# Kernel optimization log

Measured on AMD Instinct MI355X. Metric: run time of the kernel, lower is better.

## Reference

```python
import jax, jax.numpy as jnp
import numpy as np

B, S, IK, IV = 16, 2048, 3, 1
D = IK + IV          # input_size = 4
H = 256              # hidden_size
F = 512              # dim_feedforward
L = 2                # num_layers
EPS = 1e-5


def setup_inputs() -> dict:
    key = jax.random.key(0)
    ks = jax.random.split(key, 16)
    n = jax.random.normal
    inp = {
        'KEY': n(ks[0], (B, S, IK), jnp.float32),
        'VALUE': n(ks[1], (B, S, IV), jnp.float32),
        # per-layer kernel-attention projections (stacked on layer axis)
        'Wq': n(ks[2], (L, D, H), jnp.float32) * 0.1,
        'bq': jnp.zeros((L, H), jnp.float32),
        'Wk': n(ks[3], (L, D, H), jnp.float32) * 0.1,
        'bk': jnp.zeros((L, H), jnp.float32),
        'Wv': n(ks[4], (L, D, H), jnp.float32) * 0.1,
        'bv': jnp.zeros((L, H), jnp.float32),
        'Wo': n(ks[5], (L, H, D), jnp.float32) * 0.1,
        'bo': jnp.zeros((L, D), jnp.float32),
        'bw': jnp.ones((L,), jnp.float32),          # Gaussian kernel bandwidth
        # LayerNorm 1
        'g1': jnp.ones((L, D), jnp.float32),
        'be1': jnp.zeros((L, D), jnp.float32),
        # FFN
        'W1': n(ks[6], (L, D, F), jnp.float32) * 0.1,
        'b1': jnp.zeros((L, F), jnp.float32),
        'W2': n(ks[7], (L, F, D), jnp.float32) * 0.1,
        'b2': jnp.zeros((L, D), jnp.float32),
        # LayerNorm 2
        'g2': jnp.ones((L, D), jnp.float32),
        'be2': jnp.zeros((L, D), jnp.float32),
        # final fc: input_size -> input_v
        'Wfc': n(ks[8], (D, IV), jnp.float32) * 0.1,
        'bfc': jnp.zeros((IV,), jnp.float32),
    }
    return inp


def _layernorm(x, g, b):
    m = x.mean(-1, keepdims=True)
    v = ((x - m) ** 2).mean(-1, keepdims=True)
    return (x - m) * jax.lax.rsqrt(v + EPS) * g + b


def reference(KEY, VALUE, Wq, bq, Wk, bk, Wv, bv, Wo, bo, bw,
              g1, be1, W1, b1, W2, b2, g2, be2, Wfc, bfc):
    # positioning: concat coords and values -> [B, S, D]
    X = jnp.concatenate([KEY, VALUE], axis=-1)
    n_layers = Wq.shape[0]
    for i in range(n_layers):
        # Nadaraya-Watson Gaussian kernel attention (madsnn, type='nwd', kernel='gauss')
        Q = X @ Wq[i] + bq[i]                      # [B,S,H]
        K = X @ Wk[i] + bk[i]                      # [B,S,H]
        V = X @ Wv[i] + bv[i]                      # [B,S,H]
        # pairwise squared distances ||q-k||^2, [B,S,S]
        d2 = ((Q * Q).sum(-1)[:, :, None]
              + (K * K).sum(-1)[:, None, :]
              - 2.0 * jnp.einsum('bqh,bkh->bqk', Q, K))
        attn = jax.nn.softmax(-0.5 * d2 * (bw[i] ** 2), axis=-1)
        attn_out = jnp.einsum('bqk,bkh->bqh', attn, V) @ Wo[i] + bo[i]  # [B,S,D]
        # residual + LayerNorm + FFN + residual + LayerNorm (dropout = identity in eval)
        res = _layernorm(X + attn_out, g1[i], be1[i])
        ff = jax.nn.relu(res @ W1[i] + b1[i]) @ W2[i] + b2[i]
        X = _layernorm(res + ff, g2[i], be2[i])
    return X @ Wfc + bfc                            # [B,S,IV]
```

## Files before the change

### kernel.cpp

```cpp
#include <hip/hip_runtime.h>

#define BB 16
#define SS 2048
#define NTOK (BB*SS)
#define NPAIR (NTOK/2)
#define PLANE (NPAIR*4)
#define FF 512
#define EPSF 1e-5f
#define QW 8

#if __has_builtin(__builtin_amdgcn_exp2f)
#define EXP2F(x) __builtin_amdgcn_exp2f(x)
#else
#define EXP2F(x) exp2f(x)
#endif

typedef float v2f __attribute__((ext_vector_type(2)));


__device__ __forceinline__ float wred64(float v) {
#pragma unroll
  for (int m = 32; m > 0; m >>= 1) v += __shfl_xor(v, m, 64);
  return v;
}

__device__ __forceinline__ float rflf(float v) {
  union { float f; int i; } u; u.f = v;
  u.i = __builtin_amdgcn_readfirstlane(u.i);
  return u.f;
}


__global__ __launch_bounds__(64) void prep_kernel(
    const float* __restrict__ Wq, const float* __restrict__ bq,
    const float* __restrict__ Wk, const float* __restrict__ bk,
    const float* __restrict__ Wv, const float* __restrict__ bv,
    const float* __restrict__ Wo, const float* __restrict__ bw,
    const float* __restrict__ W1, const float* __restrict__ b1,
    const float* __restrict__ W2,
    float* __restrict__ sm, float* __restrict__ w1t)
{
  const int i = blockIdx.x;
  const int lane = threadIdx.x;
  float m4[4][4] = {{0}}, gkk[4][4] = {{0}}, wvo[4][4] = {{0}};
  float akk[4] = {0}, bvo[4] = {0};
  float ck1 = 0.f, ck2 = 0.f;

  for (int h = lane; h < 256; h += 64) {
    float vq[4], vk[4], vv[4], wo4[4];
#pragma unroll
    for (int a = 0; a < 4; ++a) {
      vq[a]  = Wq[(i*4 + a)*256 + h];
      vk[a]  = Wk[(i*4 + a)*256 + h];
      vv[a]  = Wv[(i*4 + a)*256 + h];
      wo4[a] = Wo[(i*256 + h)*4 + a];
    }
    const float bqh = bq[i*256 + h], bkh = bk[i*256 + h], bvh = bv[i*256 + h];
#pragma unroll
    for (int a = 0; a < 4; ++a) {
#pragma unroll
      for (int c = 0; c < 4; ++c) {
        m4[a][c]  = fmaf(vq[a], vk[c], m4[a][c]);
        gkk[a][c] = fmaf(vk[a], vk[c], gkk[a][c]);
        wvo[a][c] = fmaf(vv[a], wo4[c], wvo[a][c]);
      }
      akk[a] = fmaf(vk[a], bqh - bkh, akk[a]);
      bvo[a] = fmaf(bvh, wo4[a], bvo[a]);
    }
    ck1 = fmaf(bqh, bkh, ck1);
    ck2 = fmaf(bkh, bkh, ck2);
  }
#pragma unroll
  for (int a = 0; a < 4; ++a) {
#pragma unroll
    for (int c = 0; c < 4; ++c) {
      m4[a][c]  = wred64(m4[a][c]);
      gkk[a][c] = wred64(gkk[a][c]);
      wvo[a][c] = wred64(wvo[a][c]);
    }
    akk[a] = wred64(akk[a]);
    bvo[a] = wred64(bvo[a]);
  }
  ck1 = wred64(ck1); ck2 = wred64(ck2);

  if (lane == 0) {
    const float bwv = bw[i];
    const float bw2 = bwv * bwv * 1.44269504088896f;
    float* s = sm + i*64;
#pragma unroll
    for (int a = 0; a < 4; ++a) {
#pragma unroll
      for (int c = 0; c < 4; ++c) {
        s[a*4+c]      = bw2 * m4[a][c];
        s[16 + a*4+c] = -0.5f * bw2 * gkk[a][c];
        s[32 + a*4+c] = wvo[a][c];
      }
      s[48+a] = bw2 * akk[a];
      s[52+a] = bvo[a];
    }
    s[56] = bw2 * (ck1 - 0.5f * ck2);
  }
  for (int f = lane; f < FF; f += 64) {
    float* rec = w1t + (i*FF + f)*12;
#pragma unroll
    for (int c = 0; c < 4; ++c) rec[c]   = W1[(i*4 + c)*FF + f];
#pragma unroll
    for (int c = 0; c < 4; ++c) rec[4+c] = W2[(i*FF + f)*4 + c];
    rec[8] = b1[i*FF + f];
    rec[9] = 0.f; rec[10] = 0.f; rec[11] = 0.f;
  }
}

__device__ __forceinline__ void compute_feat(const float x[4], const float* __restrict__ s,
                                             float* __restrict__ featrec)
{
  float P[4], VT[4], tk[4];
#pragma unroll
  for (int a = 0; a < 4; ++a) {
    P[a]  = fmaf(s[a*4+3], x[3], fmaf(s[a*4+2], x[2], fmaf(s[a*4+1], x[1], s[a*4+0]*x[0])));
    tk[a] = fmaf(s[16+a*4+3], x[3], fmaf(s[16+a*4+2], x[2], fmaf(s[16+a*4+1], x[1], s[16+a*4+0]*x[0])));
    VT[a] = s[52+a] + fmaf(s[32+3*4+a], x[3], fmaf(s[32+2*4+a], x[2], fmaf(s[32+1*4+a], x[1], s[32+0*4+a]*x[0])));
  }
  float R = s[56];
#pragma unroll
  for (int a = 0; a < 4; ++a) R = fmaf(tk[a] + s[48+a], x[a], R);
  featrec[0]=P[0]; featrec[1]=P[1]; featrec[2]=P[2]; featrec[3]=P[3];
  featrec[4]=VT[0]; featrec[5]=VT[1]; featrec[6]=VT[2]; featrec[7]=VT[3];
  featrec[8]=R;
}

__global__ __launch_bounds__(256) void feat_kernel(
    const float* __restrict__ KEY, const float* __restrict__ VALUE,
    const float* __restrict__ sm, float* __restrict__ feat)
{
  const int p = blockIdx.x*256 + threadIdx.x;
  const int ta = 2*p, tb = 2*p + 1;
  float xa[4] = {KEY[ta*3], KEY[ta*3+1], KEY[ta*3+2], VALUE[ta]};
  float xb[4] = {KEY[tb*3], KEY[tb*3+1], KEY[tb*3+2], VALUE[tb]};
  float fa[9], fb[9];
  compute_feat(xa, sm, fa);
  compute_feat(xb, sm, fb);
#pragma unroll
  for (int pl = 0; pl < 4; ++pl) {
    *(float4*)(feat + (size_t)pl*PLANE + (size_t)p*4) =
        make_float4(fa[2*pl], fb[2*pl], fa[2*pl+1], fb[2*pl+1]);
  }
  *(float4*)(feat + (size_t)4*PLANE + (size_t)p*4) =
      make_float4(fa[8], fb[8], 0.f, 0.f);
}

__device__ __forceinline__ void ln4(const float t[4], const float* __restrict__ g,
                                    const float* __restrict__ b, float r[4])
{
  const float m = 0.25f*(t[0]+t[1]+t[2]+t[3]);
  const float d0 = t[0]-m, d1 = t[1]-m, d2 = t[2]-m, d3 = t[3]-m;
  const float v = 0.25f*(d0*d0 + d1*d1 + d2*d2 + d3*d3);
  const float sc = rsqrtf(v + EPSF);
  r[0] = fmaf(d0*sc, g[0], b[0]);
  r[1] = fmaf(d1*sc, g[1], b[1]);
  r[2] = fmaf(d2*sc, g[2], b[2]);
  r[3] = fmaf(d3*sc, g[3], b[3]);
}

__global__ __launch_bounds__(256, 4) void layer_kernel(
    const float* __restrict__ KEY, const float* __restrict__ VALUE,
    const float* __restrict__ X, const float* __restrict__ feat,
    const float* __restrict__ w1t, const float* __restrict__ smn,
    const float* __restrict__ bo, const float* __restrict__ g1, const float* __restrict__ be1,
    const float* __restrict__ b2v, const float* __restrict__ g2, const float* __restrict__ be2,
    float* __restrict__ Xout, float* __restrict__ featout,
    const float* __restrict__ Wfc, const float* __restrict__ bfc,
    float* __restrict__ outp, int first, int last)
{
  const int bid = blockIdx.x;
  const int b = bid >> 6, qg = bid & 63;
  const int qbase = (b << 11) + (qg << 5);
  const int tid = threadIdx.x;
  const int lane = tid & 63, wv = tid >> 6;
  const int q0 = qbase + wv*QW;

  __shared__ float sums[4*QW*9];
  __shared__ float ress[32*4];
  __shared__ float redf[8*32*4];

  float qx0[QW], qx1[QW], qx2[QW], qx3[QW];
#pragma unroll
  for (int q = 0; q < QW; ++q) {
    const int gq = q0 + q;
    float a, b_, c, d;
    if (first) {
      a = KEY[gq*3]; b_ = KEY[gq*3+1]; c = KEY[gq*3+2]; d = VALUE[gq];
    } else {
      const float4 xv = *(const float4*)(X + (size_t)gq*4);
      a = xv.x; b_ = xv.y; c = xv.z; d = xv.w;
    }
    qx0[q] = rflf(a); qx1[q] = rflf(b_); qx2[q] = rflf(c); qx3[q] = rflf(d);
  }

  v2f aV0[QW], aV1[QW], aV2[QW], aV3[QW], aD[QW];
#pragma unroll
  for (int q = 0; q < QW; ++q) {
    aV0[q] = v2f{0.f,0.f}; aV1[q] = v2f{0.f,0.f};
    aV2[q] = v2f{0.f,0.f}; aV3[q] = v2f{0.f,0.f};
    aD[q]  = v2f{0.f,0.f};
  }

  const int pb = (b << 10) + lane;
#pragma unroll 4
  for (int it = 0; it < 16; ++it) {
    const size_t o = (size_t)(pb + (it << 6)) * 4;
    const float4 A  = *(const float4*)(feat + o);
    const float4 Bf = *(const float4*)(feat + (size_t)PLANE + o);
    const float4 C  = *(const float4*)(feat + (size_t)2*PLANE + o);
    const float4 D  = *(const float4*)(feat + (size_t)3*PLANE + o);
    const float4 E  = *(const float4*)(feat + (size_t)4*PLANE + o);
    const v2f P0 = v2f{A.x, A.y},   P1 = v2f{A.z, A.w};
    const v2f P2 = v2f{Bf.x, Bf.y}, P3 = v2f{Bf.z, Bf.w};
    const v2f V0 = v2f{C.x, C.y},   V1 = v2f{C.z, C.w};
    const v2f V2 = v2f{D.x, D.y},   V3 = v2f{D.z, D.w};
    const v2f Rp = v2f{E.x, E.y};
#pragma unroll
    for (int q = 0; q < QW; ++q) {
      v2f l = __builtin_elementwise_fma(P0, v2f{qx0[q], qx0[q]}, Rp);
      l = __builtin_elementwise_fma(P1, v2f{qx1[q], qx1[q]}, l);
      l = __builtin_elementwise_fma(P2, v2f{qx2[q], qx2[q]}, l);
      l = __builtin_elementwise_fma(P3, v2f{qx3[q], qx3[q]}, l);
      const v2f e = v2f{EXP2F(l.x), EXP2F(l.y)};
      aV0[q] = __builtin_elementwise_fma(e, V0, aV0[q]);
      aV1[q] = __builtin_elementwise_fma(e, V1, aV1[q]);
      aV2[q] = __builtin_elementwise_fma(e, V2, aV2[q]);
      aV3[q] = __builtin_elementwise_fma(e, V3, aV3[q]);
      aD[q] += e;
    }
  }

  float s[QW][5];
#pragma unroll
  for (int q = 0; q < QW; ++q) {
    s[q][0] = aV0[q].x + aV0[q].y;
    s[q][1] = aV1[q].x + aV1[q].y;
    s[q][2] = aV2[q].x + aV2[q].y;
    s[q][3] = aV3[q].x + aV3[q].y;
    s[q][4] = aD[q].x + aD[q].y;
  }
#pragma unroll
  for (int q = 0; q < QW; ++q)
#pragma unroll
    for (int c = 0; c < 5; ++c) s[q][c] = wred64(s[q][c]);

  if (lane == 0) {
    float* dst = sums + wv*(QW*9);
#pragma unroll
    for (int q = 0; q < QW; ++q) {
#pragma unroll
      for (int c = 0; c < 5; ++c) dst[q*9 + c] = s[q][c];
    }
  }
  __syncthreads();

  if (tid < 32) {
    const float* sv = sums + tid*9;
    const float inv = 1.0f / sv[4];
    const int gq = qbase + tid;
    float xv0, xv1, xv2, xv3;
    if (first) {
      xv0 = KEY[gq*3]; xv1 = KEY[gq*3+1]; xv2 = KEY[gq*3+2]; xv3 = VALUE[gq];
    } else {
      const float4 xv = *(const float4*)(X + (size_t)gq*4);
      xv0 = xv.x; xv1 = xv.y; xv2 = xv.z; xv3 = xv.w;
    }
    float t4[4];
    t4[0] = xv0 + fmaf(sv[0], inv, bo[0]);
    t4[1] = xv1 + fmaf(sv[1], inv, bo[1]);
    t4[2] = xv2 + fmaf(sv[2], inv, bo[2]);
    t4[3] = xv3 + fmaf(sv[3], inv, bo[3]);
    float r[4];
    ln4(t4, g1, be1, r);
    *(float4*)(ress + tid*4) = make_float4(r[0], r[1], r[2], r[3]);
  }
  __syncthreads();

  const int tok = tid & 31, fc = tid >> 5;
  const float4 rv = *(const float4*)(ress + tok*4);
  float fa0 = 0.f, fa1 = 0.f, fa2 = 0.f, fa3 = 0.f;
  const float* wt = w1t + (size_t)fc*64*12;
#pragma unroll 4
  for (int f = 0; f < 64; ++f) {
    const float* rec = wt + f*12;
    const float4 w1r = *(const float4*)rec;
    const float4 w2r = *(const float4*)(rec + 4);
    const float b1f = rec[8];
    float h = fmaf(rv.w, w1r.w, fmaf(rv.z, w1r.z, fmaf(rv.y, w1r.y, fmaf(rv.x, w1r.x, b1f))));
    h = fmaxf(h, 0.f);
    fa0 = fmaf(h, w2r.x, fa0);
    fa1 = fmaf(h, w2r.y, fa1);
    fa2 = fmaf(h, w2r.z, fa2);
    fa3 = fmaf(h, w2r.w, fa3);
  }
  *(float4*)(redf + (size_t)((fc << 5) + tok)*4) = make_float4(fa0, fa1, fa2, fa3);
  __syncthreads();

  if (tid < 32) {
    float t2[4];
#pragma unroll
    for (int c = 0; c < 4; ++c) {
      float sa = b2v[c];
#pragma unroll
      for (int k = 0; k < 8; ++k) sa += redf[(size_t)((k << 5) + tid)*4 + c];
      t2[c] = ress[tid*4 + c] + sa;
    }
    float y[4];
    ln4(t2, g2, be2, y);
    const int gq = qbase + tid;
    if (last) {
      outp[gq] = fmaf(y[3], Wfc[3], fmaf(y[2], Wfc[2], fmaf(y[1], Wfc[1], fmaf(y[0], Wfc[0], bfc[0]))));
    } else {
      *(float4*)(Xout + (size_t)gq*4) = make_float4(y[0], y[1], y[2], y[3]);
      float fr[9];
      compute_feat(y, smn, fr);
      const int p = gq >> 1, par = gq & 1;
#pragma unroll
      for (int c = 0; c < 8; ++c)
        featout[(size_t)(c >> 1)*PLANE + (size_t)p*4 + (c & 1)*2 + par] = fr[c];
      featout[(size_t)4*PLANE + (size_t)p*4 + par] = fr[8];
    }
  }
}

extern "C" void kernel_launch(void* const* d_in, const int* in_sizes, int n_in,
                              void* d_out, int out_size, void* d_ws, size_t ws_size,
                              hipStream_t stream)
{
  const float* KEY   = (const float*)d_in[0];
  const float* VALUE = (const float*)d_in[1];
  const float* Wq  = (const float*)d_in[2];
  const float* bq  = (const float*)d_in[3];
  const float* Wk  = (const float*)d_in[4];
  const float* bk  = (const float*)d_in[5];
  const float* Wv  = (const float*)d_in[6];
  const float* bv  = (const float*)d_in[7];
  const float* Wo  = (const float*)d_in[8];
  const float* bo  = (const float*)d_in[9];
  const float* bw  = (const float*)d_in[10];
  const float* g1  = (const float*)d_in[11];
  const float* be1 = (const float*)d_in[12];
  const float* W1  = (const float*)d_in[13];
  const float* b1  = (const float*)d_in[14];
  const float* W2  = (const float*)d_in[15];
  const float* b2  = (const float*)d_in[16];
  const float* g2  = (const float*)d_in[17];
  const float* be2 = (const float*)d_in[18];
  const float* Wfc = (const float*)d_in[19];
  const float* bfc = (const float*)d_in[20];
  float* out = (float*)d_out;

  float* w    = (float*)d_ws;
  float* sm   = w;
  float* w1t  = w + 128;
  float* X1   = w + 12416;
  float* f0   = w + 143488;
  float* f1   = w + 471168;

  prep_kernel<<<2, 64, 0, stream>>>(Wq, bq, Wk, bk, Wv, bv, Wo, bw,
                                    W1, b1, W2, sm, w1t);
  feat_kernel<<<64, 256, 0, stream>>>(KEY, VALUE, sm, f0);

  layer_kernel<<<1024, 256, 0, stream>>>(KEY, VALUE, X1, f0,
      w1t, sm + 64,
      bo, g1, be1, b2, g2, be2,
      X1, f1, Wfc, bfc, out, 1, 0);

  layer_kernel<<<1024, 256, 0, stream>>>(KEY, VALUE, X1, f1,
      w1t + FF*12, sm,
      bo + 4, g1 + 4, be1 + 4, b2 + 4, g2 + 4, be2 + 4,
      X1, f1, Wfc, bfc, out, 0, 1);
}
```

Measured before the change: 187.2 us.

## Store raw key coordinates and fold projections into query side and epilogue

```diff
diff --git a/kernel.cpp b/kernel.cpp
--- a/kernel.cpp
+++ b/kernel.cpp
@@ -4,10 +4,9 @@
 #define SS 2048
 #define NTOK (BB*SS)
 #define NPAIR (NTOK/2)
-#define PLANE (NPAIR*4)
 #define FF 512
 #define EPSF 1e-5f
-#define QW 8
+#define QW 4
 
 #if __has_builtin(__builtin_amdgcn_exp2f)
 #define EXP2F(x) __builtin_amdgcn_exp2f(x)
@@ -111,42 +110,31 @@
   }
 }
 
-__device__ __forceinline__ void compute_feat(const float x[4], const float* __restrict__ s,
-                                             float* __restrict__ featrec)
-{
-  float P[4], VT[4], tk[4];
+__device__ __forceinline__ float compute_R(const float x[4], const float* __restrict__ s)
+{
+  float R = s[56];
 #pragma unroll
   for (int a = 0; a < 4; ++a) {
-    P[a]  = fmaf(s[a*4+3], x[3], fmaf(s[a*4+2], x[2], fmaf(s[a*4+1], x[1], s[a*4+0]*x[0])));
-    tk[a] = fmaf(s[16+a*4+3], x[3], fmaf(s[16+a*4+2], x[2], fmaf(s[16+a*4+1], x[1], s[16+a*4+0]*x[0])));
-    VT[a] = s[52+a] + fmaf(s[32+3*4+a], x[3], fmaf(s[32+2*4+a], x[2], fmaf(s[32+1*4+a], x[1], s[32+0*4+a]*x[0])));
-  }
-  float R = s[56];
-#pragma unroll
-  for (int a = 0; a < 4; ++a) R = fmaf(tk[a] + s[48+a], x[a], R);
-  featrec[0]=P[0]; featrec[1]=P[1]; featrec[2]=P[2]; featrec[3]=P[3];
-  featrec[4]=VT[0]; featrec[5]=VT[1]; featrec[6]=VT[2]; featrec[7]=VT[3];
-  featrec[8]=R;
+    const float tk = fmaf(s[16+a*4+3], x[3], fmaf(s[16+a*4+2], x[2],
+                     fmaf(s[16+a*4+1], x[1], s[16+a*4+0]*x[0])));
+    R = fmaf(tk + s[48+a], x[a], R);
+  }
+  return R;
 }
 
 __global__ __launch_bounds__(256) void feat_kernel(
     const float* __restrict__ KEY, const float* __restrict__ VALUE,
-    const float* __restrict__ sm, float* __restrict__ feat)
+    const float* __restrict__ sm,
+    float* __restrict__ fXA, float* __restrict__ fXB, float* __restrict__ fRR)
 {
   const int p = blockIdx.x*256 + threadIdx.x;
   const int ta = 2*p, tb = 2*p + 1;
   float xa[4] = {KEY[ta*3], KEY[ta*3+1], KEY[ta*3+2], VALUE[ta]};
   float xb[4] = {KEY[tb*3], KEY[tb*3+1], KEY[tb*3+2], VALUE[tb]};
-  float fa[9], fb[9];
-  compute_feat(xa, sm, fa);
-  compute_feat(xb, sm, fb);
-#pragma unroll
-  for (int pl = 0; pl < 4; ++pl) {
-    *(float4*)(feat + (size_t)pl*PLANE + (size_t)p*4) =
-        make_float4(fa[2*pl], fb[2*pl], fa[2*pl+1], fb[2*pl+1]);
-  }
-  *(float4*)(feat + (size_t)4*PLANE + (size_t)p*4) =
-      make_float4(fa[8], fb[8], 0.f, 0.f);
+  const float Ra = compute_R(xa, sm), Rb = compute_R(xb, sm);
+  *(float4*)(fXA + (size_t)p*4) = make_float4(xa[0], xb[0], xa[1], xb[1]);
+  *(float4*)(fXB + (size_t)p*4) = make_float4(xa[2], xb[2], xa[3], xb[3]);
+  *(v2f*)(fRR + (size_t)p*2) = v2f{Ra, Rb};
 }
 
 __device__ __forceinline__ void ln4(const float t[4], const float* __restrict__ g,
@@ -162,13 +150,15 @@
   r[3] = fmaf(d3*sc, g[3], b[3]);
 }
 
-__global__ __launch_bounds__(256, 4) void layer_kernel(
+__global__ __launch_bounds__(512, 8) void layer_kernel(
     const float* __restrict__ KEY, const float* __restrict__ VALUE,
-    const float* __restrict__ X, const float* __restrict__ feat,
-    const float* __restrict__ w1t, const float* __restrict__ smn,
+    const float* __restrict__ X,
+    const float* __restrict__ fXA, const float* __restrict__ fXB, const float* __restrict__ fRR,
+    const float* __restrict__ w1t, const float* __restrict__ smc, const float* __restrict__ smn,
     const float* __restrict__ bo, const float* __restrict__ g1, const float* __restrict__ be1,
     const float* __restrict__ b2v, const float* __restrict__ g2, const float* __restrict__ be2,
-    float* __restrict__ Xout, float* __restrict__ featout,
+    float* __restrict__ Xout,
+    float* __restrict__ foXA, float* __restrict__ foXB, float* __restrict__ foRR,
     const float* __restrict__ Wfc, const float* __restrict__ bfc,
     float* __restrict__ outp, int first, int last)
 {
@@ -179,88 +169,108 @@
   const int lane = tid & 63, wv = tid >> 6;
   const int q0 = qbase + wv*QW;
 
-  __shared__ float sums[4*QW*9];
-  __shared__ float ress[32*4];
-  __shared__ float redf[8*32*4];
-
-  float qx0[QW], qx1[QW], qx2[QW], qx3[QW];
+  __shared__ float smem[5120];
+  float* sXA = smem;
+  float* sXB = smem + 2048;
+  float* sRR = smem + 4096;
+  float* sums = smem;
+  float* ress = smem + 256;
+  float* redf = smem + 512;
+
+  float gv0[QW], gv1[QW], gv2[QW], gv3[QW];
 #pragma unroll
   for (int q = 0; q < QW; ++q) {
     const int gq = q0 + q;
-    float a, b_, c, d;
+    float x0, x1, x2, x3;
     if (first) {
-      a = KEY[gq*3]; b_ = KEY[gq*3+1]; c = KEY[gq*3+2]; d = VALUE[gq];
+      x0 = KEY[gq*3]; x1 = KEY[gq*3+1]; x2 = KEY[gq*3+2]; x3 = VALUE[gq];
     } else {
       const float4 xv = *(const float4*)(X + (size_t)gq*4);
-      a = xv.x; b_ = xv.y; c = xv.z; d = xv.w;
-    }
-    qx0[q] = rflf(a); qx1[q] = rflf(b_); qx2[q] = rflf(c); qx3[q] = rflf(d);
-  }
-
-  v2f aV0[QW], aV1[QW], aV2[QW], aV3[QW], aD[QW];
+      x0 = xv.x; x1 = xv.y; x2 = xv.z; x3 = xv.w;
+    }
+    float g0 = fmaf(smc[12], x3, fmaf(smc[ 8], x2, fmaf(smc[4], x1, smc[0]*x0)));
+    float g1_ = fmaf(smc[13], x3, fmaf(smc[ 9], x2, fmaf(smc[5], x1, smc[1]*x0)));
+    float g2_ = fmaf(smc[14], x3, fmaf(smc[10], x2, fmaf(smc[6], x1, smc[2]*x0)));
+    float g3_ = fmaf(smc[15], x3, fmaf(smc[11], x2, fmaf(smc[7], x1, smc[3]*x0)));
+    gv0[q] = rflf(g0); gv1[q] = rflf(g1_); gv2[q] = rflf(g2_); gv3[q] = rflf(g3_);
+  }
+
+  v2f aX0[QW], aX1[QW], aX2[QW], aX3[QW], aD[QW];
 #pragma unroll
   for (int q = 0; q < QW; ++q) {
-    aV0[q] = v2f{0.f,0.f}; aV1[q] = v2f{0.f,0.f};
-    aV2[q] = v2f{0.f,0.f}; aV3[q] = v2f{0.f,0.f};
+    aX0[q] = v2f{0.f,0.f}; aX1[q] = v2f{0.f,0.f};
+    aX2[q] = v2f{0.f,0.f}; aX3[q] = v2f{0.f,0.f};
     aD[q]  = v2f{0.f,0.f};
   }
 
-  const int pb = (b << 10) + lane;
-#pragma unroll 4
-  for (int it = 0; it < 16; ++it) {
-    const size_t o = (size_t)(pb + (it << 6)) * 4;
-    const float4 A  = *(const float4*)(feat + o);
-    const float4 Bf = *(const float4*)(feat + (size_t)PLANE + o);
-    const float4 C  = *(const float4*)(feat + (size_t)2*PLANE + o);
-    const float4 D  = *(const float4*)(feat + (size_t)3*PLANE + o);
-    const float4 E  = *(const float4*)(feat + (size_t)4*PLANE + o);
-    const v2f P0 = v2f{A.x, A.y},   P1 = v2f{A.z, A.w};
-    const v2f P2 = v2f{Bf.x, Bf.y}, P3 = v2f{Bf.z, Bf.w};
-    const v2f V0 = v2f{C.x, C.y},   V1 = v2f{C.z, C.w};
-    const v2f V2 = v2f{D.x, D.y},   V3 = v2f{D.z, D.w};
-    const v2f Rp = v2f{E.x, E.y};
+  const int pbb = b << 10;
+#pragma unroll
+  for (int c = 0; c < 2; ++c) {
+    {
+      const int gp = pbb + c*512 + tid;
+      const float4 va = *(const float4*)(fXA + (size_t)gp*4);
+      const float4 vb = *(const float4*)(fXB + (size_t)gp*4);
+      const v2f    vr = *(const v2f*)(fRR + (size_t)gp*2);
+      __syncthreads();
+      *(float4*)(sXA + tid*4) = va;
+      *(float4*)(sXB + tid*4) = vb;
+      *(v2f*)(sRR + tid*2) = vr;
+      __syncthreads();
+    }
+#pragma unroll 2
+    for (int it = 0; it < 8; ++it) {
+      const int p = lane + (it << 6);
+      const float4 XAv = *(const float4*)(sXA + p*4);
+      const float4 XBv = *(const float4*)(sXB + p*4);
+      const v2f   RRv = *(const v2f*)(sRR + p*2);
+      const v2f X0 = v2f{XAv.x, XAv.y}, X1 = v2f{XAv.z, XAv.w};
+      const v2f X2 = v2f{XBv.x, XBv.y}, X3 = v2f{XBv.z, XBv.w};
+#pragma unroll
+      for (int q = 0; q < QW; ++q) {
+        v2f l = __builtin_elementwise_fma(X0, v2f{gv0[q], gv0[q]}, RRv);
+        l = __builtin_elementwise_fma(X1, v2f{gv1[q], gv1[q]}, l);
+        l = __builtin_elementwise_fma(X2, v2f{gv2[q], gv2[q]}, l);
+        l = __builtin_elementwise_fma(X3, v2f{gv3[q], gv3[q]}, l);
+        const v2f e = v2f{EXP2F(l.x), EXP2F(l.y)};
+        aX0[q] = __builtin_elementwise_fma(e, X0, aX0[q]);
+        aX1[q] = __builtin_elementwise_fma(e, X1, aX1[q]);
+        aX2[q] = __builtin_elementwise_fma(e, X2, aX2[q]);
+        aX3[q] = __builtin_elementwise_fma(e, X3, aX3[q]);
+        aD[q] += e;
+      }
+    }
+  }
+  __syncthreads();
+
+  {
+    float s[QW][5];
 #pragma unroll
     for (int q = 0; q < QW; ++q) {
-      v2f l = __builtin_elementwise_fma(P0, v2f{qx0[q], qx0[q]}, Rp);
-      l = __builtin_elementwise_fma(P1, v2f{qx1[q], qx1[q]}, l);
-      l = __builtin_elementwise_fma(P2, v2f{qx2[q], qx2[q]}, l);
-      l = __builtin_elementwise_fma(P3, v2f{qx3[q], qx3[q]}, l);
-      const v2f e = v2f{EXP2F(l.x), EXP2F(l.y)};
-      aV0[q] = __builtin_elementwise_fma(e, V0, aV0[q]);
-      aV1[q] = __builtin_elementwise_fma(e, V1, aV1[q]);
-      aV2[q] = __builtin_elementwise_fma(e, V2, aV2[q]);
-      aV3[q] = __builtin_elementwise_fma(e, V3, aV3[q]);
-      aD[q] += e;
-    }
-  }
-
-  float s[QW][5];
-#pragma unroll
-  for (int q = 0; q < QW; ++q) {
-    s[q][0] = aV0[q].x + aV0[q].y;
-    s[q][1] = aV1[q].x + aV1[q].y;
-    s[q][2] = aV2[q].x + aV2[q].y;
-    s[q][3] = aV3[q].x + aV3[q].y;
-    s[q][4] = aD[q].x + aD[q].y;
-  }
-#pragma unroll
-  for (int q = 0; q < QW; ++q)
-#pragma unroll
-    for (int c = 0; c < 5; ++c) s[q][c] = wred64(s[q][c]);
-
-  if (lane == 0) {
-    float* dst = sums + wv*(QW*9);
-#pragma unroll
-    for (int q = 0; q < QW; ++q) {
-#pragma unroll
-      for (int c = 0; c < 5; ++c) dst[q*9 + c] = s[q][c];
+      s[q][0] = aX0[q].x + aX0[q].y;
+      s[q][1] = aX1[q].x + aX1[q].y;
+      s[q][2] = aX2[q].x + aX2[q].y;
+      s[q][3] = aX3[q].x + aX3[q].y;
+      s[q][4] = aD[q].x + aD[q].y;
+    }
+#pragma unroll
+    for (int q = 0; q < QW; ++q)
+#pragma unroll
+      for (int c = 0; c < 5; ++c) s[q][c] = wred64(s[q][c]);
+    if (lane == 0) {
+#pragma unroll
+      for (int q = 0; q < QW; ++q) {
+        float* dst = sums + (wv*QW + q)*6;
+#pragma unroll
+        for (int c = 0; c < 5; ++c) dst[c] = s[q][c];
+      }
     }
   }
   __syncthreads();
 
   if (tid < 32) {
-    const float* sv = sums + tid*9;
+    const float* sv = sums + tid*6;
     const float inv = 1.0f / sv[4];
+    const float m0 = sv[0]*inv, m1 = sv[1]*inv, m2 = sv[2]*inv, m3 = sv[3]*inv;
     const int gq = qbase + tid;
     float xv0, xv1, xv2, xv3;
     if (first) {
@@ -270,10 +280,16 @@
       xv0 = xv.x; xv1 = xv.y; xv2 = xv.z; xv3 = xv.w;
     }
     float t4[4];
-    t4[0] = xv0 + fmaf(sv[0], inv, bo[0]);
-    t4[1] = xv1 + fmaf(sv[1], inv, bo[1]);
-    t4[2] = xv2 + fmaf(sv[2], inv, bo[2]);
-    t4[3] = xv3 + fmaf(sv[3], inv, bo[3]);
+#pragma unroll
+    for (int a = 0; a < 4; ++a) {
+      float at = smc[52+a];
+      at = fmaf(smc[32+0*4+a], m0, at);
+      at = fmaf(smc[32+1*4+a], m1, at);
+      at = fmaf(smc[32+2*4+a], m2, at);
+      at = fmaf(smc[32+3*4+a], m3, at);
+      const float xr = (a==0) ? xv0 : (a==1) ? xv1 : (a==2) ? xv2 : xv3;
+      t4[a] = xr + at + bo[a];
+    }
     float r[4];
     ln4(t4, g1, be1, r);
     *(float4*)(ress + tid*4) = make_float4(r[0], r[1], r[2], r[3]);
@@ -283,9 +299,9 @@
   const int tok = tid & 31, fc = tid >> 5;
   const float4 rv = *(const float4*)(ress + tok*4);
   float fa0 = 0.f, fa1 = 0.f, fa2 = 0.f, fa3 = 0.f;
-  const float* wt = w1t + (size_t)fc*64*12;
+  const float* wt = w1t + (size_t)fc*32*12;
 #pragma unroll 4
-  for (int f = 0; f < 64; ++f) {
+  for (int f = 0; f < 32; ++f) {
     const float* rec = wt + f*12;
     const float4 w1r = *(const float4*)rec;
     const float4 w2r = *(const float4*)(rec + 4);
@@ -306,7 +322,7 @@
     for (int c = 0; c < 4; ++c) {
       float sa = b2v[c];
 #pragma unroll
-      for (int k = 0; k < 8; ++k) sa += redf[(size_t)((k << 5) + tid)*4 + c];
+      for (int k = 0; k < 16; ++k) sa += redf[(size_t)((k << 5) + tid)*4 + c];
       t2[c] = ress[tid*4 + c] + sa;
     }
     float y[4];
@@ -316,13 +332,13 @@
       outp[gq] = fmaf(y[3], Wfc[3], fmaf(y[2], Wfc[2], fmaf(y[1], Wfc[1], fmaf(y[0], Wfc[0], bfc[0]))));
     } else {
       *(float4*)(Xout + (size_t)gq*4) = make_float4(y[0], y[1], y[2], y[3]);
-      float fr[9];
-      compute_feat(y, smn, fr);
+      const float Rn = compute_R(y, smn);
       const int p = gq >> 1, par = gq & 1;
-#pragma unroll
-      for (int c = 0; c < 8; ++c)
-        featout[(size_t)(c >> 1)*PLANE + (size_t)p*4 + (c & 1)*2 + par] = fr[c];
-      featout[(size_t)4*PLANE + (size_t)p*4 + par] = fr[8];
+      foXA[(size_t)p*4 + par]     = y[0];
+      foXA[(size_t)p*4 + 2 + par] = y[1];
+      foXB[(size_t)p*4 + par]     = y[2];
+      foXB[(size_t)p*4 + 2 + par] = y[3];
+      foRR[(size_t)p*2 + par]     = Rn;
     }
   }
 }
@@ -358,20 +374,24 @@
   float* sm   = w;
   float* w1t  = w + 128;
   float* X1   = w + 12416;
-  float* f0   = w + 143488;
-  float* f1   = w + 471168;
+  float* f0XA = w + 143488;
+  float* f0XB = w + 209024;
+  float* f0RR = w + 274560;
+  float* f1XA = w + 307328;
+  float* f1XB = w + 372864;
+  float* f1RR = w + 438400;
 
   prep_kernel<<<2, 64, 0, stream>>>(Wq, bq, Wk, bk, Wv, bv, Wo, bw,
                                     W1, b1, W2, sm, w1t);
-  feat_kernel<<<64, 256, 0, stream>>>(KEY, VALUE, sm, f0);
-
-  layer_kernel<<<1024, 256, 0, stream>>>(KEY, VALUE, X1, f0,
-      w1t, sm + 64,
+  feat_kernel<<<64, 256, 0, stream>>>(KEY, VALUE, sm, f0XA, f0XB, f0RR);
+
+  layer_kernel<<<1024, 512, 0, stream>>>(KEY, VALUE, X1, f0XA, f0XB, f0RR,
+      w1t, sm, sm + 64,
       bo, g1, be1, b2, g2, be2,
-      X1, f1, Wfc, bfc, out, 1, 0);
-
-  layer_kernel<<<1024, 256, 0, stream>>>(KEY, VALUE, X1, f1,
-      w1t + FF*12, sm,
+      X1, f1XA, f1XB, f1RR, Wfc, bfc, out, 1, 0);
+
+  layer_kernel<<<1024, 512, 0, stream>>>(KEY, VALUE, X1, f1XA, f1XB, f1RR,
+      w1t + FF*12, sm + 64, sm,
       bo + 4, g1 + 4, be1 + 4, b2 + 4, g2 + 4, be2 + 4,
-      X1, f1, Wfc, bfc, out, 0, 1);
-}
+      X1, f1XA, f1XB, f1RR, Wfc, bfc, out, 0, 1);
+}
```

New measurement: 162.2 us, median of 2. -13.4%, faster.
